# Performance work log

Measured on AMD Instinct MI355X. Metric: run time of the kernel, lower is better.

## Reference

```python
import jax, jax.numpy as jnp
import numpy as np

FP8_MAX = 448.0  # max normal of float8_e4m3fn
NUM_HEADS = 16


def act_quant(x):
    # per-tensor fp8 quantization: scale so max|x| maps to FP8_MAX
    scale = jnp.max(jnp.abs(x)) / FP8_MAX
    q = (x / scale).astype(jnp.float8_e4m3fn)
    return q, scale


def setup_inputs() -> dict:
    key = jax.random.key(0)
    k1, k2, k3, k4 = jax.random.split(key, 4)
    B, S, H = 2, 2048, 2048
    x = jax.random.normal(k1, (B, S, H), dtype=jnp.float32)
    W_qkv = jax.random.normal(k2, (H, 3 * H), dtype=jnp.float32) * (1.0 / np.sqrt(H))
    W_out = jax.random.normal(k3, (H, H), dtype=jnp.float32) * (1.0 / np.sqrt(H))
    b_out = jnp.zeros((H,), dtype=jnp.float32)
    return {"x": x, "W_qkv": W_qkv, "W_out": W_out, "b_out": b_out}


def reference(x, W_qkv, W_out, b_out):
    B, S, H = x.shape
    nH = NUM_HEADS
    hd = H // nH  # 128, matches head_dim default used for scaling

    qkv = jnp.einsum('bsh,hf->bsf', x, W_qkv)          # [B,S,3H]
    qkv = qkv.reshape(B, S, 3, nH, hd)
    q = qkv[:, :, 0].transpose(0, 2, 1, 3)             # [B,nH,S,hd]
    k = qkv[:, :, 1].transpose(0, 2, 1, 3)
    v = qkv[:, :, 2].transpose(0, 2, 1, 3)

    q8, q_scale = act_quant(q)
    k8, k_scale = act_quant(k)
    # fp8_gemm_optimized: dequantized GEMM = (a @ b) * a_scale * b_scale
    scores = jnp.einsum('bhqd,bhkd->bhqk',
                        q8.astype(jnp.float32), k8.astype(jnp.float32))
    scores = scores * (q_scale * k_scale) / jnp.sqrt(jnp.float32(hd))

    attn = jax.nn.softmax(scores, axis=-1)             # [B,nH,S,S]
    # (dropout omitted: deterministic / eval mode)

    v8, v_scale = act_quant(v)
    out = jnp.einsum('bhqk,bhkd->bhqd', attn, v8.astype(jnp.float32))
    out = out * v_scale                                # a_scale = 1 for attn weights

    out = out.transpose(0, 2, 1, 3).reshape(B, S, H)
    return jnp.einsum('bsh,ho->bso', out, W_out) + b_out
```

## Files before the change

### kernel.cpp

```cpp
#include <hip/hip_runtime.h>
#include <hip/hip_bf16.h>
#include <math.h>

#define B_   2
#define S_   2048
#define H_   2048
#define NH   16
#define HD   128
#define ROWS (B_ * S_)
#define F3   (3 * H_)
#define KS   2048

typedef _Float16 f16x8 __attribute__((ext_vector_type(8)));
typedef float    f32x4  __attribute__((ext_vector_type(4)));
typedef float    f32x16 __attribute__((ext_vector_type(16)));

union H2 { unsigned u; _Float16 h[2]; };
union H4 { ushort4 s4; _Float16 h[4]; };
union PU { unsigned u[4]; f16x8 v8; };

__device__ __forceinline__ void gl_lds16(const void* g, void* l) {
  __builtin_amdgcn_global_load_lds(
      (const __attribute__((address_space(1))) void*)g,
      (__attribute__((address_space(3))) void*)l, 16, 0, 0);
}

__device__ __forceinline__ float quant_e4m3(float x) {
  float ax = fabsf(x);
  float q;
  if (ax < 0.015625f) {
    q = rintf(ax * 512.0f) * (1.0f / 512.0f);
  } else {
    unsigned eb = __float_as_uint(ax) & 0x7f800000u;
    float quantum = __uint_as_float(eb - (3u << 23));
    q = rintf(ax / quantum) * quantum;
    if (q > 448.0f) q = 448.0f;
  }
  return copysignf(q, x);
}

__global__ __launch_bounds__(256) void split_ab(
    const float* __restrict__ in, _Float16* __restrict__ hi,
    _Float16* __restrict__ lo) {
  const size_t i = (size_t)blockIdx.x * 256 + threadIdx.x;
  float4 v = ((const float4*)in)[i];
  H4 h, l;
  h.h[0] = (_Float16)v.x; l.h[0] = (_Float16)(v.x - (float)h.h[0]);
  h.h[1] = (_Float16)v.y; l.h[1] = (_Float16)(v.y - (float)h.h[1]);
  h.h[2] = (_Float16)v.z; l.h[2] = (_Float16)(v.z - (float)h.h[2]);
  h.h[3] = (_Float16)v.w; l.h[3] = (_Float16)(v.w - (float)h.h[3]);
  ((ushort4*)hi)[i] = h.s4;
  ((ushort4*)lo)[i] = l.s4;
}

__global__ __launch_bounds__(256) void split_tr(
    const float* __restrict__ in, _Float16* __restrict__ hi,
    _Float16* __restrict__ lo, int K, int N) {
  __shared__ _Float16 ht[64][72];
  __shared__ _Float16 lt[64][72];
  const int t = threadIdx.x;
  const int n0 = blockIdx.x * 64, k0 = blockIdx.y * 64;
#pragma unroll
  for (int p = 0; p < 4; p++) {
    const int k = p * 16 + (t >> 4);
    const int n = (t & 15) * 4;
    float4 v = *(const float4*)(in + (size_t)(k0 + k) * N + n0 + n);
    _Float16 h0 = (_Float16)v.x, h1 = (_Float16)v.y,
             h2 = (_Float16)v.z, h3 = (_Float16)v.w;
    ht[n + 0][k] = h0; lt[n + 0][k] = (_Float16)(v.x - (float)h0);
    ht[n + 1][k] = h1; lt[n + 1][k] = (_Float16)(v.y - (float)h1);
    ht[n + 2][k] = h2; lt[n + 2][k] = (_Float16)(v.z - (float)h2);
    ht[n + 3][k] = h3; lt[n + 3][k] = (_Float16)(v.w - (float)h3);
  }
  __syncthreads();
#pragma unroll
  for (int it = 0; it < 2; it++) {
    const int idx = it * 256 + t;
    const int r = idx >> 3, c = (idx & 7) * 8;
    *(uint4*)(hi + (size_t)(n0 + r) * K + k0 + c) = *(const uint4*)&ht[r][c];
    *(uint4*)(lo + (size_t)(n0 + r) * K + k0 + c) = *(const uint4*)&lt[r][c];
  }
}

#define STAGE_A(tt, dst) do {                                                  \
    const _Float16* As_ = ((tt) < 64) ? Ahi : Alo;                             \
    const size_t sb_ = (size_t)(row0 + wave * 8 + srow) * KS +                 \
                       (((tt) & 31) << 6) + schunk;                            \
    _Float16* db_ = (dst) + wave * 512;                                        \
    gl_lds16(As_ + sb_,                    db_);                               \
    gl_lds16(As_ + sb_ + (size_t)64 * KS,  db_ + 4096);                        \
    gl_lds16(As_ + sb_ + (size_t)128 * KS, db_ + 8192);                       \
    gl_lds16(As_ + sb_ + (size_t)192 * KS, db_ + 12288);                       \
  } while (0)

#define STAGE_B(tt, dst) do {                                                  \
    const _Float16* Bs_ = ((((tt) >> 5)) == 1) ? Btlo : Bthi;                  \
    const size_t sb_ = (size_t)(col0 + wave * 8 + srow) * KS +                 \
                       (((tt) & 31) << 6) + schunk;                            \
    _Float16* db_ = (dst) + 16384 + wave * 512;                                \
    gl_lds16(Bs_ + sb_,                    db_);                               \
    gl_lds16(Bs_ + sb_ + (size_t)64 * KS,  db_ + 4096);                        \
  } while (0)

__global__ __launch_bounds__(512, 2) void gemm_split256(
    const _Float16* __restrict__ Ahi, const _Float16* __restrict__ Alo,
    const _Float16* __restrict__ Bthi, const _Float16* __restrict__ Btlo,
    float* __restrict__ C, const float* __restrict__ bias,
    unsigned* mx, int N, int has_bias) {
  __shared__ __align__(16) _Float16 lds[73728];
  const int t = threadIdx.x;
  const int wave = t >> 6, lane = t & 63;
  const int l15 = lane & 15, g = lane >> 4;
  const int wm = wave >> 1, wn = wave & 1;

  const int gx = gridDim.x;
  const int nwg = gx * gridDim.y;
  const int bid = blockIdx.y * gx + blockIdx.x;
  const int tile = (bid & 7) * (nwg >> 3) + (bid >> 3);
  const int row0 = (tile / gx) * 256, col0 = (tile % gx) * 128;

  const int srow = lane >> 3;
  const int schunk = ((lane & 7) ^ srow) << 3;

  f32x4 acc[4][4] = {};

  _Float16* bufA = lds;
  _Float16* bufB = lds + 24576;
  _Float16* bufC = lds + 49152;

  STAGE_A(0, bufA);
  STAGE_B(0, bufA);
  STAGE_A(1, bufB);
  STAGE_B(1, bufB);
  asm volatile("s_waitcnt vmcnt(6)" ::: "memory");
  __builtin_amdgcn_s_barrier();

  for (int kc = 0; kc < 96; kc++) {
    const _Float16* Ab = bufA;
    const _Float16* Bb = bufA + 16384;
    f16x8 af0[4], bf0[4], af1[4], bf1[4];
#pragma unroll
    for (int i = 0; i < 4; i++) {
      const int r_ = wm * 64 + i * 16 + l15;
      af0[i] = *(const f16x8*)(Ab + r_ * 64 + ((g ^ (r_ & 7)) << 3));
      af1[i] = *(const f16x8*)(Ab + r_ * 64 + (((4 ^ g) ^ (r_ & 7)) << 3));
    }
#pragma unroll
    for (int j = 0; j < 4; j++) {
      const int r_ = wn * 64 + j * 16 + l15;
      bf0[j] = *(const f16x8*)(Bb + r_ * 64 + ((g ^ (r_ & 7)) << 3));
      bf1[j] = *(const f16x8*)(Bb + r_ * 64 + (((4 ^ g) ^ (r_ & 7)) << 3));
    }
    if (kc + 2 < 96) {
      STAGE_A(kc + 2, bufC);
      STAGE_B(kc + 2, bufC);
    }
#pragma unroll
    for (int i = 0; i < 4; i++)
#pragma unroll
      for (int j = 0; j < 4; j++)
        acc[i][j] = __builtin_amdgcn_mfma_f32_16x16x32_f16(af0[i], bf0[j], acc[i][j], 0, 0, 0);
#pragma unroll
    for (int i = 0; i < 4; i++)
#pragma unroll
      for (int j = 0; j < 4; j++)
        acc[i][j] = __builtin_amdgcn_mfma_f32_16x16x32_f16(af1[i], bf1[j], acc[i][j], 0, 0, 0);
    if (kc < 94) { asm volatile("s_waitcnt vmcnt(6)" ::: "memory"); }
    else         { asm volatile("s_waitcnt vmcnt(0)" ::: "memory"); }
    __builtin_amdgcn_s_barrier();
    _Float16* tmp = bufA; bufA = bufB; bufB = bufC; bufC = tmp;
  }

  float bmax = 0.0f;
#pragma unroll
  for (int j = 0; j < 4; j++) {
    const int col = col0 + wn * 64 + j * 16 + l15;
    const float bv = has_bias ? bias[col] : 0.0f;
#pragma unroll
    for (int i = 0; i < 4; i++) {
      const int rbase = row0 + wm * 64 + i * 16 + g * 4;
#pragma unroll
      for (int r = 0; r < 4; r++) {
        const float v = acc[i][j][r] + bv;
        C[(size_t)(rbase + r) * N + col] = v;
        bmax = fmaxf(bmax, fabsf(v));
      }
    }
  }

  if (mx) {
    __syncthreads();
    float* red = (float*)lds;
    red[t] = bmax;
    __syncthreads();
    for (int s2 = 256; s2 > 0; s2 >>= 1) {
      if (t < s2) red[t] = fmaxf(red[t], red[t + s2]);
      __syncthreads();
    }
    if (t == 0) atomicMax(mx + (col0 >> 11), __float_as_uint(red[0]));
  }
}

__global__ __launch_bounds__(256) void quant_qkv(
    const float* __restrict__ qkv, const unsigned* __restrict__ mx,
    _Float16* __restrict__ q8, _Float16* __restrict__ k8,
    _Float16* __restrict__ v8t) {
  __shared__ _Float16 tile[64 * 72];
  const int t = threadIdx.x;
  const int bid = blockIdx.x;

  if (bid < 16384) {
    const size_t base = ((size_t)bid * 256 + t) * 4;
    const int row = (int)(base >> 12);
    const int col = (int)(base & 4095);
    const int seg = col >> 11;
    const int c2 = col & 2047;
    const int h = c2 >> 7, d = c2 & 127;
    const int b = row >> 11, s = row & 2047;
    const float scale = __uint_as_float(mx[seg]) / 448.0f;
    float4 v = *(const float4*)(qkv + (size_t)row * F3 + col);
    H4 r;
    r.h[0] = (_Float16)quant_e4m3(v.x / scale);
    r.h[1] = (_Float16)quant_e4m3(v.y / scale);
    r.h[2] = (_Float16)quant_e4m3(v.z / scale);
    r.h[3] = (_Float16)quant_e4m3(v.w / scale);
    _Float16* dst = seg ? k8 : q8;
    const size_t di = ((size_t)((b * NH + h) * S_) + s) * HD + d;
    *(ushort4*)(dst + di) = r.s4;
  } else {
    const int bt = bid - 16384;
    const int dtile = bt & 1;
    const int stile = (bt >> 1) & 31;
    const int bh = bt >> 6;
    const int b = bh >> 4, h = bh & 15;
    const int s0 = stile * 64, d0 = dtile * 64;
    const float scale = __uint_as_float(mx[2]) / 448.0f;

#pragma unroll
    for (int r = 0; r < 4; r++) {
      const int s = s0 + r * 16 + (t >> 4);
      const int dl = (t & 15) * 4;
      float4 v = *(const float4*)(qkv + (size_t)(b * S_ + s) * F3 + 4096 + h * HD + d0 + dl);
      tile[(dl + 0) * 72 + r * 16 + (t >> 4)] = (_Float16)quant_e4m3(v.x / scale);
      tile[(dl + 1) * 72 + r * 16 + (t >> 4)] = (_Float16)quant_e4m3(v.y / scale);
      tile[(dl + 2) * 72 + r * 16 + (t >> 4)] = (_Float16)quant_e4m3(v.z / scale);
      tile[(dl + 3) * 72 + r * 16 + (t >> 4)] = (_Float16)quant_e4m3(v.w / scale);
    }
    __syncthreads();
#pragma unroll
    for (int j = 0; j < 2; j++) {
      const int wi = j * 256 + t;
      const int dl = wi >> 3;
      const int sch = (wi & 7) * 8;
      uint4 val = *(const uint4*)(tile + dl * 72 + sch);
      *(uint4*)(v8t + (size_t)bh * (HD * S_) + (size_t)(d0 + dl) * S_ + s0 + sch) = val;
    }
  }
}

__global__ __launch_bounds__(256, 2) void attn_kernel(
    const _Float16* __restrict__ q8, const _Float16* __restrict__ k8,
    const _Float16* __restrict__ v8t, const unsigned* __restrict__ mx,
    _Float16* __restrict__ oHi, _Float16* __restrict__ oLo) {
  __shared__ __align__(16) char ldsb[65536];

  const int t = threadIdx.x;
  const int wave = t >> 6;
  const int lane = t & 63;
  const int l31 = lane & 31;
  const int hf = lane >> 5;

  const int qt = blockIdx.x & 15;
  const int bh = blockIdx.x >> 4;
  const int b = bh >> 4, h = bh & 15;
  const int q0 = qt * 128 + wave * 32;

  const float qs = __uint_as_float(mx[0]) * (1.0f / 448.0f);
  const float ks = __uint_as_float(mx[1]) * (1.0f / 448.0f);
  const float vs = __uint_as_float(mx[2]) * (1.0f / 448.0f);
  const float sfac = qs * ks * 0.08838834764831843f;

  f16x8 qf[8];
  {
    const _Float16* qp = q8 + ((size_t)(bh * S_) + q0 + l31) * HD + hf * 8;
#pragma unroll
    for (int st = 0; st < 8; st++)
      qf[st] = *(const f16x8*)(qp + st * 16);
  }

  f32x16 acc[4] = {};
  float m_base = 0.0f;
  float l_run = 0.0f;

  const size_t kB_ = (size_t)(bh * S_) * HD;
  const size_t vB_ = (size_t)bh * (HD * S_);
  const int k_key = t >> 4;
  const int k_dch = (t & 15) * 8;
  const int k_wch = (((t & 15) ^ (k_key & 7)) << 3);
  const int v_d   = t >> 3;
  const int v_sch = (t & 7) * 8;
  const int v_wch = (((t & 7) ^ (v_d & 7)) << 3);

  const int NT = S_ / 64;
  uint4 kp[4], vp[4];

#pragma unroll
  for (int r = 0; r < 4; r++)
    kp[r] = *(const uint4*)(k8 + kB_ + (size_t)(r * 16 + k_key) * HD + k_dch);
#pragma unroll
  for (int r = 0; r < 4; r++)
    vp[r] = *(const uint4*)(v8t + vB_ + (size_t)(r * 32 + v_d) * S_ + v_sch);
  {
    _Float16* K0 = (_Float16*)ldsb;
    _Float16* V0 = (_Float16*)(ldsb + 32768);
#pragma unroll
    for (int r = 0; r < 4; r++)
      *(uint4*)(K0 + (r * 16 + k_key) * 128 + k_wch) = kp[r];
#pragma unroll
    for (int r = 0; r < 4; r++)
      *(uint4*)(V0 + (r * 32 + v_d) * 64 + v_wch) = vp[r];
  }
#pragma unroll
  for (int r = 0; r < 4; r++)
    kp[r] = *(const uint4*)(k8 + kB_ + (size_t)(64 + r * 16 + k_key) * HD + k_dch);
#pragma unroll
  for (int r = 0; r < 4; r++)
    vp[r] = *(const uint4*)(v8t + vB_ + (size_t)(r * 32 + v_d) * S_ + 64 + v_sch);
  __syncthreads();

  for (int kt = 0; kt < NT; kt++) {
    const _Float16* Klds  = (const _Float16*)(ldsb + (kt & 1) * 16384);
    const _Float16* VTlds = (const _Float16*)(ldsb + 32768 + (kt & 1) * 16384);
    if (kt + 1 < NT) {
      _Float16* Kn = (_Float16*)(ldsb + ((kt + 1) & 1) * 16384);
      _Float16* Vn = (_Float16*)(ldsb + 32768 + ((kt + 1) & 1) * 16384);
#pragma unroll
      for (int r = 0; r < 4; r++)
        *(uint4*)(Kn + (r * 16 + k_key) * 128 + k_wch) = kp[r];
#pragma unroll
      for (int r = 0; r < 4; r++)
        *(uint4*)(Vn + (r * 32 + v_d) * 64 + v_wch) = vp[r];
    }
    if (kt + 2 < NT) {
      const int nk = (kt + 2) * 64;
#pragma unroll
      for (int r = 0; r < 4; r++)
        kp[r] = *(const uint4*)(k8 + kB_ + (size_t)(nk + r * 16 + k_key) * HD + k_dch);
#pragma unroll
      for (int r = 0; r < 4; r++)
        vp[r] = *(const uint4*)(v8t + vB_ + (size_t)(r * 32 + v_d) * S_ + nk + v_sch);
    }

#pragma unroll
    for (int sub = 0; sub < 2; sub++) {
      const int ksub = sub * 32;
      f32x16 s = {};
      __builtin_amdgcn_s_setprio(1);
#pragma unroll
      for (int st = 0; st < 8; st++) {
        const int krow = ksub + l31;
        f16x8 af = *(const f16x8*)(Klds + krow * 128 +
                                   (((st * 2 + hf) ^ (krow & 7)) << 3));
        s = __builtin_amdgcn_mfma_f32_32x32x16_f16(af, qf[st], s, 0, 0, 0);
      }
      __builtin_amdgcn_s_setprio(0);
      f16x8 vf0 = *(const f16x8*)(VTlds + l31 * 64 +
                                  (((sub * 4 + 0 * 2 + hf) ^ (l31 & 7)) << 3));
      f16x8 vf1 = *(const f16x8*)(VTlds + l31 * 64 +
                                  (((sub * 4 + 1 * 2 + hf) ^ (l31 & 7)) << 3));
      float p[16];
      if (kt == 0 && sub == 0) {
        float tmax = -3.0e38f;
#pragma unroll
        for (int i = 0; i < 16; i++) {
          p[i] = s[i] * sfac;
          tmax = fmaxf(tmax, p[i]);
        }
        tmax = fmaxf(tmax, __shfl_xor(tmax, 32));
        m_base = tmax;
        float rs = 0.0f;
#pragma unroll
        for (int i = 0; i < 16; i++) {
          p[i] = __expf(p[i] - tmax);
          rs += p[i];
        }
        l_run += rs;
      } else {
        const float mb = m_base;
        float rs = 0.0f;
#pragma unroll
        for (int i = 0; i < 16; i++) {
          p[i] = fminf(__expf(fmaf(s[i], sfac, -mb)), 60000.0f);
          rs += p[i];
        }
        l_run += rs;
      }
      f16x8 pf[2];
#pragma unroll
      for (int c = 0; c < 2; c++) {
        const int c8 = c * 8;
        const int sidx = hf ? 0 : 4;
        const int oidx = hf ? 4 : 0;
        H2 s0h, s1h, o0h, o1h;
        s0h.h[0] = (_Float16)p[c8 + sidx];     s0h.h[1] = (_Float16)p[c8 + sidx + 1];
        s1h.h[0] = (_Float16)p[c8 + sidx + 2]; s1h.h[1] = (_Float16)p[c8 + sidx + 3];
        o0h.h[0] = (_Float16)p[c8 + oidx];     o0h.h[1] = (_Float16)p[c8 + oidx + 1];
        o1h.h[0] = (_Float16)p[c8 + oidx + 2]; o1h.h[1] = (_Float16)p[c8 + oidx + 3];
        unsigned r0 = (unsigned)__shfl_xor((int)s0h.u, 32);
        unsigned r1 = (unsigned)__shfl_xor((int)s1h.u, 32);
        PU pu;
        if (hf == 0) { pu.u[0] = o0h.u; pu.u[1] = o1h.u; pu.u[2] = r0; pu.u[3] = r1; }
        else         { pu.u[0] = r0;    pu.u[1] = r1;    pu.u[2] = o0h.u; pu.u[3] = o1h.u; }
        pf[c] = pu.v8;
      }
#pragma unroll
      for (int dt = 0; dt < 4; dt++) {
        f16x8 nf0, nf1;
        if (dt < 3) {
          const int vrow = (dt + 1) * 32 + l31;
          nf0 = *(const f16x8*)(VTlds + vrow * 64 +
                                (((sub * 4 + 0 * 2 + hf) ^ (vrow & 7)) << 3));
          nf1 = *(const f16x8*)(VTlds + vrow * 64 +
                                (((sub * 4 + 1 * 2 + hf) ^ (vrow & 7)) << 3));
        }
        __builtin_amdgcn_s_setprio(1);
        acc[dt] = __builtin_amdgcn_mfma_f32_32x32x16_f16(vf0, pf[0], acc[dt], 0, 0, 0);
        acc[dt] = __builtin_amdgcn_mfma_f32_32x32x16_f16(vf1, pf[1], acc[dt], 0, 0, 0);
        __builtin_amdgcn_s_setprio(0);
        vf0 = nf0; vf1 = nf1;
      }
    }
    __syncthreads();
  }

  l_run += __shfl_xor(l_run, 32);

  float* scr = (float*)ldsb + wave * 1056;
  const float f = vs / l_run;
#pragma unroll
  for (int dt = 0; dt < 4; dt++) {
#pragma unroll
    for (int i = 0; i < 16; i++) {
      const int dl = (i & 3) + 8 * (i >> 2) + 4 * hf;
      scr[dl * 33 + l31] = acc[dt][i] * f;
    }
    __syncthreads();
#pragma unroll
    for (int g = 0; g < 4; g++) {
      const int idx = g * 64 + lane;
      const int ql = idx >> 3;
      const int dd = (idx & 7) * 4;
      float4 o;
      o.x = scr[(dd + 0) * 33 + ql];
      o.y = scr[(dd + 1) * 33 + ql];
      o.z = scr[(dd + 2) * 33 + ql];
      o.w = scr[(dd + 3) * 33 + ql];
      H4 hh, ll;
      hh.h[0] = (_Float16)o.x; ll.h[0] = (_Float16)(o.x - (float)hh.h[0]);
      hh.h[1] = (_Float16)o.y; ll.h[1] = (_Float16)(o.y - (float)hh.h[1]);
      hh.h[2] = (_Float16)o.z; ll.h[2] = (_Float16)(o.z - (float)hh.h[2]);
      hh.h[3] = (_Float16)o.w; ll.h[3] = (_Float16)(o.w - (float)hh.h[3]);
      const int qg = q0 + ql;
      const size_t ofs = (size_t)(b * S_ + qg) * H_ + h * HD + dt * 32 + dd;
      *(ushort4*)(oHi + ofs) = hh.s4;
      *(ushort4*)(oLo + ofs) = ll.s4;
    }
    __syncthreads();
  }
}

extern "C" void kernel_launch(void* const* d_in, const int* in_sizes, int n_in,
                              void* d_out, int out_size, void* d_ws, size_t ws_size,
                              hipStream_t stream) {
  const float* x     = (const float*)d_in[0];
  const float* W_qkv = (const float*)d_in[1];
  const float* W_out = (const float*)d_in[2];
  const float* b_out = (const float*)d_in[3];
  float* out = (float*)d_out;

  char* ws = (char*)d_ws;
  float*    qkv    = (float*)ws;
  _Float16* A2hi   = (_Float16*)(ws + 33554432);
  _Float16* A2lo   = (_Float16*)(ws + 50331648);
  _Float16* B2thi  = (_Float16*)(ws + 67108864);
  _Float16* B2tlo  = (_Float16*)(ws + 75497472);
  _Float16* B1thi  = (_Float16*)(ws + 100663296);
  _Float16* B1tlo  = (_Float16*)(ws + 125829120);
  _Float16* q8     = (_Float16*)(ws + 100663296);
  _Float16* k8     = (_Float16*)(ws + 117440512);
  _Float16* v8t    = (_Float16*)(ws + 134217728);
  _Float16* A1hi   = (_Float16*)(ws + 150994944);
  _Float16* A1lo   = (_Float16*)(ws + 167772160);
  unsigned* mx     = (unsigned*)(ws + 184549376);

  hipMemsetAsync(mx, 0, 3 * sizeof(unsigned), stream);

  split_ab<<<(ROWS * H_) / 1024, 256, 0, stream>>>(x, A1hi, A1lo);
  split_tr<<<dim3(F3 / 64, H_ / 64), 256, 0, stream>>>(W_qkv, B1thi, B1tlo, H_, F3);

  gemm_split256<<<dim3(F3 / 128, ROWS / 256), 512, 0, stream>>>(
      A1hi, A1lo, B1thi, B1tlo, qkv, nullptr, mx, F3, 0);

  quant_qkv<<<16384 + B_ * NH * 32 * 2, 256, 0, stream>>>(qkv, mx, q8, k8, v8t);

  attn_kernel<<<B_ * NH * 16, 256, 0, stream>>>(q8, k8, v8t, mx, A2hi, A2lo);

  split_tr<<<dim3(H_ / 64, H_ / 64), 256, 0, stream>>>(W_out, B2thi, B2tlo, H_, H_);

  gemm_split256<<<dim3(H_ / 128, ROWS / 256), 512, 0, stream>>>(
      A2hi, A2lo, B2thi, B2tlo, out, b_out, nullptr, H_, 1);
}
```

Before: 805.8 us.

## Restructure split-fp16 GEMM into 4-buffer K32 pipeline with fragment prefetch

Changes the GEMM main loop from a 3-buffer, K=64 per step pipeline to a 4-buffer, K=32 per step pipeline staged three steps ahead. LDS fragments for the next step are read into a second register set while the current MFMAs run, so LDS read latency overlaps compute. LDS usage drops from 144KB to 96KB per block. The cost is twice as many barriers and waitcnt points per K, smaller loads per stage, and more registers for the double fragment set.

New measurement: 794.7 us. No clear change (-1.4%).

```diff
diff --git a/kernel.cpp b/kernel.cpp
--- a/kernel.cpp
+++ b/kernel.cpp
@@ -10,6 +10,7 @@
 #define ROWS (B_ * S_)
 #define F3   (3 * H_)
 #define KS   2048
+#define NKC  192
 
 typedef _Float16 f16x8 __attribute__((ext_vector_type(8)));
 typedef float    f32x4  __attribute__((ext_vector_type(4)));
@@ -18,6 +19,8 @@
 union H2 { unsigned u; _Float16 h[2]; };
 union H4 { ushort4 s4; _Float16 h[4]; };
 union PU { unsigned u[4]; f16x8 v8; };
+
+struct FragSet { f16x8 a[4]; f16x8 b[4]; };
 
 __device__ __forceinline__ void gl_lds16(const void* g, void* l) {
   __builtin_amdgcn_global_load_lds(
@@ -82,24 +85,57 @@
   }
 }
 
-#define STAGE_A(tt, dst) do {                                                  \
-    const _Float16* As_ = ((tt) < 64) ? Ahi : Alo;                             \
-    const size_t sb_ = (size_t)(row0 + wave * 8 + srow) * KS +                 \
-                       (((tt) & 31) << 6) + schunk;                            \
-    _Float16* db_ = (dst) + wave * 512;                                        \
-    gl_lds16(As_ + sb_,                    db_);                               \
-    gl_lds16(As_ + sb_ + (size_t)64 * KS,  db_ + 4096);                        \
-    gl_lds16(As_ + sb_ + (size_t)128 * KS, db_ + 8192);                       \
-    gl_lds16(As_ + sb_ + (size_t)192 * KS, db_ + 12288);                       \
+#define ABUF(i) (lds + (i) * 12288)
+
+#define STAGE32(tt, dstA) do {                                                 \
+    const _Float16* As_ = ((tt) < 128) ? Ahi : Alo;                            \
+    const _Float16* Bs_ = ((((tt) >> 6)) == 1) ? Btlo : Bthi;                  \
+    const int koff_ = ((tt) & 63) << 5;                                        \
+    {                                                                          \
+      const int c0_ = t, r0_ = c0_ >> 2, cl0_ = c0_ & 3;                       \
+      gl_lds16(As_ + (size_t)(row0 + r0_) * KS + koff_ + ((cl0_ ^ (r0_ & 3)) << 3), \
+               (dstA) + c0_ * 8);                                              \
+      const int c1_ = 512 + t, r1_ = c1_ >> 2, cl1_ = c1_ & 3;                 \
+      gl_lds16(As_ + (size_t)(row0 + r1_) * KS + koff_ + ((cl1_ ^ (r1_ & 3)) << 3), \
+               (dstA) + c1_ * 8);                                              \
+      const int cb_ = t, rb_ = cb_ >> 2, clb_ = cb_ & 3;                       \
+      gl_lds16(Bs_ + (size_t)(col0 + rb_) * KS + koff_ + ((clb_ ^ (rb_ & 3)) << 3), \
+               (dstA) + 8192 + cb_ * 8);                                       \
+    }                                                                          \
   } while (0)
 
-#define STAGE_B(tt, dst) do {                                                  \
-    const _Float16* Bs_ = ((((tt) >> 5)) == 1) ? Btlo : Bthi;                  \
-    const size_t sb_ = (size_t)(col0 + wave * 8 + srow) * KS +                 \
-                       (((tt) & 31) << 6) + schunk;                            \
-    _Float16* db_ = (dst) + 16384 + wave * 512;                                \
-    gl_lds16(Bs_ + sb_,                    db_);                               \
-    gl_lds16(Bs_ + sb_ + (size_t)64 * KS,  db_ + 4096);                        \
+#define READ_FRAGS(bi, FR) do {                                                \
+    const _Float16* Ab_ = ABUF(bi);                                            \
+    const _Float16* Bb_ = Ab_ + 8192;                                          \
+    _Pragma("unroll")                                                          \
+    for (int i_ = 0; i_ < 4; i_++) {                                           \
+      const int r_ = wm * 64 + i_ * 16 + l15;                                  \
+      (FR).a[i_] = *(const f16x8*)(Ab_ + r_ * 32 + ((g ^ (r_ & 3)) << 3));     \
+    }                                                                          \
+    _Pragma("unroll")                                                          \
+    for (int j_ = 0; j_ < 4; j_++) {                                           \
+      const int r_ = wn * 64 + j_ * 16 + l15;                                  \
+      (FR).b[j_] = *(const f16x8*)(Bb_ + r_ * 32 + ((g ^ (r_ & 3)) << 3));     \
+    }                                                                          \
+  } while (0)
+
+#define MFMA16(FR) do {                                                        \
+    _Pragma("unroll")                                                          \
+    for (int i_ = 0; i_ < 4; i_++)                                             \
+      _Pragma("unroll")                                                        \
+      for (int j_ = 0; j_ < 4; j_++)                                           \
+        acc[i_][j_] = __builtin_amdgcn_mfma_f32_16x16x32_f16(                  \
+            (FR).a[i_], (FR).b[j_], acc[i_][j_], 0, 0, 0);                     \
+  } while (0)
+
+#define BODY(u, kcv, FRc, FRn) do {                                            \
+    const int kc_ = (kcv);                                                     \
+    if (kc_ + 3 < NKC) STAGE32(kc_ + 3, ABUF(((u) + 3) & 3));                  \
+    if (kc_ + 1 < NKC) READ_FRAGS(((u) + 1) & 3, FRn);                         \
+    MFMA16(FRc);                                                               \
+    if (kc_ < NKC - 3) { asm volatile("s_waitcnt vmcnt(3)" ::: "memory"); }    \
+    else               { asm volatile("s_waitcnt vmcnt(0)" ::: "memory"); }    \
+    __builtin_amdgcn_s_barrier();                                              \
   } while (0)
 
 __global__ __launch_bounds__(512, 2) void gemm_split256(
@@ -107,7 +143,7 @@
     const _Float16* __restrict__ Bthi, const _Float16* __restrict__ Btlo,
     float* __restrict__ C, const float* __restrict__ bias,
     unsigned* mx, int N, int has_bias) {
-  __shared__ __align__(16) _Float16 lds[73728];
+  __shared__ __align__(16) _Float16 lds[49152];
   const int t = threadIdx.x;
   const int wave = t >> 6, lane = t & 63;
   const int l15 = lane & 15, g = lane >> 4;
@@ -119,56 +155,22 @@
   const int tile = (bid & 7) * (nwg >> 3) + (bid >> 3);
   const int row0 = (tile / gx) * 256, col0 = (tile % gx) * 128;
 
-  const int srow = lane >> 3;
-  const int schunk = ((lane & 7) ^ srow) << 3;
-
   f32x4 acc[4][4] = {};
-
-  _Float16* bufA = lds;
-  _Float16* bufB = lds + 24576;
-  _Float16* bufC = lds + 49152;
-
-  STAGE_A(0, bufA);
-  STAGE_B(0, bufA);
-  STAGE_A(1, bufB);
-  STAGE_B(1, bufB);
-  asm volatile("s_waitcnt vmcnt(6)" ::: "memory");
+  FragSet fr0, fr1;
+
+  STAGE32(0, ABUF(0));
+  STAGE32(1, ABUF(1));
+  STAGE32(2, ABUF(2));
+  asm volatile("s_waitcnt vmcnt(3)" ::: "memory");
   __builtin_amdgcn_s_barrier();
-
-  for (int kc = 0; kc < 96; kc++) {
-    const _Float16* Ab = bufA;
-    const _Float16* Bb = bufA + 16384;
-    f16x8 af0[4], bf0[4], af1[4], bf1[4];
-#pragma unroll
-    for (int i = 0; i < 4; i++) {
-      const int r_ = wm * 64 + i * 16 + l15;
-      af0[i] = *(const f16x8*)(Ab + r_ * 64 + ((g ^ (r_ & 7)) << 3));
-      af1[i] = *(const f16x8*)(Ab + r_ * 64 + (((4 ^ g) ^ (r_ & 7)) << 3));
-    }
-#pragma unroll
-    for (int j = 0; j < 4; j++) {
-      const int r_ = wn * 64 + j * 16 + l15;
-      bf0[j] = *(const f16x8*)(Bb + r_ * 64 + ((g ^ (r_ & 7)) << 3));
-      bf1[j] = *(const f16x8*)(Bb + r_ * 64 + (((4 ^ g) ^ (r_ & 7)) << 3));
-    }
-    if (kc + 2 < 96) {
-      STAGE_A(kc + 2, bufC);
-      STAGE_B(kc + 2, bufC);
-    }
-#pragma unroll
-    for (int i = 0; i < 4; i++)
-#pragma unroll
-      for (int j = 0; j < 4; j++)
-        acc[i][j] = __builtin_amdgcn_mfma_f32_16x16x32_f16(af0[i], bf0[j], acc[i][j], 0, 0, 0);
-#pragma unroll
-    for (int i = 0; i < 4; i++)
-#pragma unroll
-      for (int j = 0; j < 4; j++)
-        acc[i][j] = __builtin_amdgcn_mfma_f32_16x16x32_f16(af1[i], bf1[j], acc[i][j], 0, 0, 0);
-    if (kc < 94) { asm volatile("s_waitcnt vmcnt(6)" ::: "memory"); }
-    else         { asm volatile("s_waitcnt vmcnt(0)" ::: "memory"); }
-    __builtin_amdgcn_s_barrier();
-    _Float16* tmp = bufA; bufA = bufB; bufB = bufC; bufC = tmp;
+  READ_FRAGS(0, fr0);
+
+  for (int grp = 0; grp < NKC / 4; grp++) {
+    const int base = grp * 4;
+    BODY(0, base + 0, fr0, fr1);
+    BODY(1, base + 1, fr1, fr0);
+    BODY(2, base + 2, fr0, fr1);
+    BODY(3, base + 3, fr1, fr0);
   }
 
   float bmax = 0.0f;
```
